# Kernel tuning notes

Measured on AMD Instinct MI355X. Metric: run time of the kernel, lower is better.

Reference implementation:

```python
import jax, jax.numpy as jnp
import numpy as np

B, T, D = 128, 32, 1024
ADA, INTER, RANK = 1024, 1024, 8
LN_EPS = 1e-5

def setup_inputs() -> dict:
    key = jax.random.key(0)
    ks = jax.random.split(key, 9)
    return {
        "x": jax.random.normal(ks[0], (B, T, D), dtype=jnp.float32),
        "ada_emb": jax.random.normal(ks[1], (B, ADA), dtype=jnp.float32),
        "base_layer": jax.random.normal(ks[2], (D, D), dtype=jnp.float32),  # torch.randn init
        "w1": jax.random.normal(ks[3], (ADA, INTER), dtype=jnp.float32) * 0.02,
        "b1": jnp.zeros((INTER,), dtype=jnp.float32),
        "w2": jax.random.normal(ks[4], (INTER, 2 * D * RANK), dtype=jnp.float32) * 0.02,
        "b2": jnp.zeros((2 * D * RANK,), dtype=jnp.float32),
        "ln_g": jnp.ones((ADA,), dtype=jnp.float32),
        "ln_b": jnp.zeros((ADA,), dtype=jnp.float32),
    }

def _layernorm(x, g, b):
    mu = jnp.mean(x, axis=-1, keepdims=True)
    var = jnp.var(x, axis=-1, keepdims=True)
    return (x - mu) * jax.lax.rsqrt(var + LN_EPS) * g + b

def reference(x, ada_emb, base_layer, w1, b1, w2, b2, ln_g, ln_b):
    b, t, d = x.shape
    # hypernetwork: cond -> per-sample LoRA factors
    ae = _layernorm(ada_emb, ln_g, ln_b)
    h = jax.nn.gelu(ae @ w1 + b1, approximate=False)  # nn.GELU is exact (erf)
    xw = h @ w2 + b2                                   # (B, 2*D*rank)
    x_a, x_b = jnp.split(xw, 2, axis=-1)
    x_a = x_a.reshape(b, d, RANK)
    x_b = x_b.reshape(b, d, RANK)
    # fused per-sample weight: base + x_a @ x_b^T  -> (B, D, D)
    layer = base_layer[None, :, :] + jnp.einsum('bdr,bkr->bdk', x_a, x_b)
    # apply shared per-sample weight to every token (equiv to repeat_interleave + bmm)
    out = jnp.einsum('btc,bco->bto', x, layer)
    return x + out  # residual=True
```

## Files before the change

### kernel.cpp

```cpp
#include <hip/hip_runtime.h>
#include <hip/hip_bf16.h>
#include <math.h>

#define BB    128
#define TT    32
#define DD    1024
#define NADA  1024
#define NINT  1024
#define NRANK 8
#define LNEPS 1e-5f
#define SPLITS 8
#define TKCH  8

using bf16x8 = __attribute__((ext_vector_type(8))) short;
using f32x4  = __attribute__((ext_vector_type(4))) float;

__device__ __forceinline__ short f2bf(float f) {
    __hip_bfloat16 h = __float2bfloat16(f);
    return *reinterpret_cast<short*>(&h);
}

__device__ __forceinline__ void async16(const void* g, void* l) {
    __builtin_amdgcn_global_load_lds(
        (const __attribute__((address_space(1))) void*)g,
        (__attribute__((address_space(3))) void*)l, 16, 0, 0);
}

__global__ __launch_bounds__(256) void ln_kernel(
    const float* __restrict__ ada, const float* __restrict__ g,
    const float* __restrict__ beta, short* __restrict__ ae)
{
    const int b = blockIdx.x;
    const float* row = ada + (size_t)b * NADA;
    float sum = 0.f, sumsq = 0.f;
    for (int i = threadIdx.x; i < NADA; i += 256) {
        float v = row[i];
        sum += v; sumsq += v * v;
    }
    #pragma unroll
    for (int off = 32; off > 0; off >>= 1) {
        sum   += __shfl_down(sum, off);
        sumsq += __shfl_down(sumsq, off);
    }
    __shared__ float s1[4], s2[4];
    const int wid = threadIdx.x >> 6, lane = threadIdx.x & 63;
    if (lane == 0) { s1[wid] = sum; s2[wid] = sumsq; }
    __syncthreads();
    if (threadIdx.x == 0) {
        float a = 0.f, c = 0.f;
        for (int i = 0; i < 4; ++i) { a += s1[i]; c += s2[i]; }
        s1[0] = a; s2[0] = c;
    }
    __syncthreads();
    const float mu  = s1[0] * (1.f / NADA);
    const float var = s2[0] * (1.f / NADA) - mu * mu;
    const float inv = rsqrtf(var + LNEPS);
    for (int i = threadIdx.x; i < NADA; i += 256) {
        ae[(size_t)b * NADA + i] = f2bf((row[i] - mu) * inv * g[i] + beta[i]);
    }
}

__global__ __launch_bounds__(256) void cast_kernel(
    const float* __restrict__ in, short* __restrict__ out)
{
    const int idx = blockIdx.x * 256 + threadIdx.x;
    float4 v = reinterpret_cast<const float4*>(in)[idx];
    short4 p;
    p.x = f2bf(v.x); p.y = f2bf(v.y); p.z = f2bf(v.z); p.w = f2bf(v.w);
    reinterpret_cast<short4*>(out)[idx] = p;
}

template <bool ADDI>
__global__ __launch_bounds__(256) void tcast_kernel(
    const float* __restrict__ in, short* __restrict__ out, int K, int N)
{
    __shared__ float t[64][68];
    const int n0 = blockIdx.x * 64, k0 = blockIdx.y * 64;
    const int tid = threadIdx.x;
    #pragma unroll
    for (int it = 0; it < 4; ++it) {
        const int idx = it * 256 + tid;
        const int r = idx >> 4, c4 = (idx & 15) * 4;
        float4 v = *(const float4*)(in + (size_t)(k0 + r) * N + n0 + c4);
        t[r][c4 + 0] = v.x; t[r][c4 + 1] = v.y;
        t[r][c4 + 2] = v.z; t[r][c4 + 3] = v.w;
    }
    __syncthreads();
    #pragma unroll
    for (int it = 0; it < 4; ++it) {
        const int idx = it * 256 + tid;
        const int rn = idx >> 4, c4 = (idx & 15) * 4;
        short4 p;
        float f0 = t[c4 + 0][rn], f1 = t[c4 + 1][rn];
        float f2 = t[c4 + 2][rn], f3 = t[c4 + 3][rn];
        if (ADDI) {
            const int n = n0 + rn;
            if (k0 + c4 + 0 == n) f0 += 1.f;
            if (k0 + c4 + 1 == n) f1 += 1.f;
            if (k0 + c4 + 2 == n) f2 += 1.f;
            if (k0 + c4 + 3 == n) f3 += 1.f;
        }
        p.x = f2bf(f0); p.y = f2bf(f1); p.z = f2bf(f2); p.w = f2bf(f3);
        *(short4*)(out + (size_t)(n0 + rn) * K + k0 + c4) = p;
    }
}

template <int BM, int BN, int WM, int WN, int EPI>
__global__ __launch_bounds__(256, 2) void mgemm(
    const short* __restrict__ A, const short* __restrict__ Bt,
    const float* __restrict__ bias, float* __restrict__ C,
    int M, int N, int K, int kLen,
    const float* __restrict__ tmat, const float* __restrict__ xw)
{
    constexpr int MT = BM / WM / 16;
    constexpr int NT = BN / WN / 16;
    constexpr int LA = BM / 64;
    constexpr int LB = BN / 64;

    __shared__ __align__(16) short As[BM * 32];
    __shared__ __align__(16) short Bs[BN * 32];
    __shared__ float tmS[(EPI == 2) ? BM * 8 : 1];
    __shared__ float xbS[(EPI == 2) ? (BM / 32) * BN * 8 : 1];

    const int bm = blockIdx.y * BM;
    const int bn = blockIdx.x * BN;
    const int kStart = blockIdx.z * kLen;
    const int tid = threadIdx.x;
    const int wave = tid >> 6, lane = tid & 63;
    const int wm0 = (wave / WN) * (BM / WM);
    const int wn0 = (wave % WN) * (BN / WN);
    const int quad = lane >> 4, r16 = lane & 15;

    if constexpr (EPI == 2) {
        const int b0 = bm >> 5;
        #pragma unroll
        for (int s = 0; s < BM * 8 / 1024; ++s) {
            const int i4 = s * 256 + tid;
            *(float4*)&tmS[i4 * 4] = *(const float4*)(tmat + (size_t)bm * 8 + i4 * 4);
        }
        const int grp = tid >> 6;
        const int inner = tid & 63;
        const float* src = xw + (size_t)(b0 + grp) * (2 * DD * NRANK) + DD * NRANK
                              + (size_t)bn * 8;
        *(float4*)&xbS[grp * BN * 8 + inner * 8]     = *(const float4*)(src + inner * 8);
        *(float4*)&xbS[grp * BN * 8 + inner * 8 + 4] = *(const float4*)(src + inner * 8 + 4);
    }

    f32x4 acc[MT][NT] = {};

    for (int kt = 0; kt < kLen; kt += 32) {
        const int k0 = kStart + kt;
        #pragma unroll
        for (int s = 0; s < LA; ++s) {
            const int c = s * 256 + tid;
            async16(A + (size_t)(bm + (c >> 2)) * K + k0 + (c & 3) * 8, &As[c * 8]);
        }
        #pragma unroll
        for (int s = 0; s < LB; ++s) {
            const int c = s * 256 + tid;
            async16(Bt + (size_t)(bn + (c >> 2)) * K + k0 + (c & 3) * 8, &Bs[c * 8]);
        }
        __syncthreads();
        bf16x8 af[MT], bfr[NT];
        #pragma unroll
        for (int i = 0; i < MT; ++i)
            af[i] = *reinterpret_cast<const bf16x8*>(&As[(wm0 + i * 16 + r16) * 32 + quad * 8]);
        #pragma unroll
        for (int j = 0; j < NT; ++j)
            bfr[j] = *reinterpret_cast<const bf16x8*>(&Bs[(wn0 + j * 16 + r16) * 32 + quad * 8]);
        #pragma unroll
        for (int i = 0; i < MT; ++i)
            #pragma unroll
            for (int j = 0; j < NT; ++j)
                acc[i][j] = __builtin_amdgcn_mfma_f32_16x16x32_bf16(
                    af[i], bfr[j], acc[i][j], 0, 0, 0);
        __syncthreads();
    }

    if constexpr (EPI == 2) {
        float xbr[NT][8];
        #pragma unroll
        for (int j = 0; j < NT; ++j) {
            const int nl = wn0 + j * 16 + r16;
            (void)nl;
        }
        #pragma unroll
        for (int i = 0; i < MT; ++i) {
            const int mlBase = wm0 + i * 16 + quad * 4;
            const int s = mlBase >> 5;
            #pragma unroll
            for (int j = 0; j < NT; ++j) {
                const int nl = wn0 + j * 16 + r16;
                #pragma unroll
                for (int rr = 0; rr < 8; ++rr)
                    xbr[j][rr] = xbS[(s * BN + nl) * 8 + rr];
            }
            #pragma unroll
            for (int r = 0; r < 4; ++r) {
                const int ml = mlBase + r;
                const int m = bm + ml;
                float t8[8];
                #pragma unroll
                for (int rr = 0; rr < 8; ++rr) t8[rr] = tmS[ml * 8 + rr];
                #pragma unroll
                for (int j = 0; j < NT; ++j) {
                    const int n = bn + wn0 + j * 16 + r16;
                    float v = acc[i][j][r];
                    #pragma unroll
                    for (int rr = 0; rr < 8; ++rr) v += t8[rr] * xbr[j][rr];
                    C[(size_t)m * N + n] = v;
                }
            }
        }
    } else {
        #pragma unroll
        for (int i = 0; i < MT; ++i) {
            #pragma unroll
            for (int r = 0; r < 4; ++r) {
                const int m = bm + wm0 + i * 16 + quad * 4 + r;
                #pragma unroll
                for (int j = 0; j < NT; ++j) {
                    const int n = bn + wn0 + j * 16 + r16;
                    float v = acc[i][j][r];
                    if (EPI == 0) {
                        C[((size_t)blockIdx.z * M + m) * N + n] = v;
                    } else {
                        C[(size_t)m * N + n] = v + bias[n];
                    }
                }
            }
        }
    }
}

__global__ __launch_bounds__(256) void combine_gelu(
    const float* __restrict__ part, const float* __restrict__ b1,
    short* __restrict__ h)
{
    const int idx = blockIdx.x * 256 + threadIdx.x;
    float s = b1[idx & (NINT - 1)];
    #pragma unroll
    for (int z = 0; z < SPLITS; ++z) s += part[(size_t)z * BB * NINT + idx];
    s = 0.5f * s * (1.f + erff(s * 0.70710678118654752f));
    h[idx] = f2bf(s);
}

__global__ __launch_bounds__(256) void tpart_kernel(
    const float* __restrict__ x, const float* __restrict__ xw,
    float* __restrict__ tp)
{
    __shared__ float xa[(DD / TKCH) * NRANK];
    const int b = blockIdx.x, ch = blockIdx.y;
    const float* src = xw + (size_t)b * (2 * DD * NRANK) + (size_t)ch * (DD / TKCH) * NRANK;
    float4 v = *(const float4*)(src + threadIdx.x * 4);
    *(float4*)(xa + threadIdx.x * 4) = v;
    __syncthreads();
    const int m = threadIdx.x >> 3;
    const int r = threadIdx.x & 7;
    const float* xrow = x + ((size_t)b * TT + m) * DD + ch * (DD / TKCH);
    float accv = 0.f;
    #pragma unroll 4
    for (int c = 0; c < DD / TKCH; c += 4) {
        float4 xr = *(const float4*)(xrow + c);
        accv += xr.x * xa[(c + 0) * NRANK + r];
        accv += xr.y * xa[(c + 1) * NRANK + r];
        accv += xr.z * xa[(c + 2) * NRANK + r];
        accv += xr.w * xa[(c + 3) * NRANK + r];
    }
    tp[((size_t)ch * BB * TT + (size_t)b * TT + m) * NRANK + r] = accv;
}

__global__ __launch_bounds__(256) void tcomb_kernel(
    const float* __restrict__ tp, float* __restrict__ tm)
{
    const int i = blockIdx.x * 256 + threadIdx.x;
    float s = 0.f;
    #pragma unroll
    for (int ch = 0; ch < TKCH; ++ch) s += tp[(size_t)ch * BB * TT * NRANK + i];
    tm[i] = s;
}

extern "C" void kernel_launch(void* const* d_in, const int* in_sizes, int n_in,
                              void* d_out, int out_size, void* d_ws, size_t ws_size,
                              hipStream_t stream)
{
    const float* x    = (const float*)d_in[0];
    const float* ada  = (const float*)d_in[1];
    const float* base = (const float*)d_in[2];
    const float* w1   = (const float*)d_in[3];
    const float* b1   = (const float*)d_in[4];
    const float* w2   = (const float*)d_in[5];
    const float* b2   = (const float*)d_in[6];
    const float* lng  = (const float*)d_in[7];
    const float* lnb  = (const float*)d_in[8];
    float* out = (float*)d_out;

    char* w = (char*)d_ws;
    short* x_bf  = (short*)w;  w += (size_t)8 << 20;
    short* w2t   = (short*)w;  w += (size_t)32 << 20;
    short* w1t   = (short*)w;  w += (size_t)2 << 20;
    short* baset = (short*)w;  w += (size_t)2 << 20;
    short* ae_bf = (short*)w;  w += (size_t)256 << 10;
    short* h_bf  = (short*)w;  w += (size_t)256 << 10;
    float* xw    = (float*)w;  w += (size_t)8 << 20;
    float* tm    = (float*)w;  w += (size_t)128 << 10;
    float* part  = (float*)w;
    float* tp    = part;

    cast_kernel<<<BB * TT * DD / 1024, 256, 0, stream>>>(x, x_bf);
    tcast_kernel<false><<<dim3(NINT / 64, NADA / 64), 256, 0, stream>>>(w1, w1t, NADA, NINT);
    tcast_kernel<true><<<dim3(DD / 64, DD / 64), 256, 0, stream>>>(base, baset, DD, DD);
    tcast_kernel<false><<<dim3(2 * DD * NRANK / 64, NINT / 64), 256, 0, stream>>>(
        w2, w2t, NINT, 2 * DD * NRANK);
    ln_kernel<<<BB, 256, 0, stream>>>(ada, lng, lnb, ae_bf);
    mgemm<64, 64, 2, 2, 0><<<dim3(NINT / 64, BB / 64, SPLITS), 256, 0, stream>>>(
        ae_bf, w1t, nullptr, part, BB, NINT, NADA, NADA / SPLITS, nullptr, nullptr);
    combine_gelu<<<BB * NINT / 256, 256, 0, stream>>>(part, b1, h_bf);
    mgemm<64, 64, 2, 2, 1><<<dim3(2 * DD * NRANK / 64, BB / 64, 1), 256, 0, stream>>>(
        h_bf, w2t, b2, xw, BB, 2 * DD * NRANK, NINT, NINT, nullptr, nullptr);
    tpart_kernel<<<dim3(BB, TKCH), 256, 0, stream>>>(x, xw, tp);
    tcomb_kernel<<<BB * TT * NRANK / 256, 256, 0, stream>>>(tp, tm);
    mgemm<128, 64, 2, 2, 2><<<dim3(DD / 64, BB * TT / 128, 1), 256, 0, stream>>>(
        x_bf, baset, nullptr, out, BB * TT, DD, DD, DD, tm, xw);
}
```

Baseline: 197.8 us.

## Fuse prep kernels, drop split-K for first GEMM, fold combines into GEMM epilogues

Merges the x cast, three transposed weight casts and layernorm into a single block-indexed prep kernel. The first GEMM no longer uses split-K; bias and exact GELU are applied in its epilogue, so the combine_gelu pass goes away. The tcomb reduction is moved into the prologue of the final GEMM, which sums the eight partials itself. The aim is fewer launches and less intermediate traffic, at the cost of the first GEMM running only 32 blocks over the full K.

```diff
diff --git a/kernel.cpp b/kernel.cpp
--- a/kernel.cpp
+++ b/kernel.cpp
@@ -9,7 +9,6 @@
 #define NINT  1024
 #define NRANK 8
 #define LNEPS 1e-5f
-#define SPLITS 8
 #define TKCH  8
 
 using bf16x8 = __attribute__((ext_vector_type(8))) short;
@@ -26,57 +25,11 @@
         (__attribute__((address_space(3))) void*)l, 16, 0, 0);
 }
 
-__global__ __launch_bounds__(256) void ln_kernel(
-    const float* __restrict__ ada, const float* __restrict__ g,
-    const float* __restrict__ beta, short* __restrict__ ae)
-{
-    const int b = blockIdx.x;
-    const float* row = ada + (size_t)b * NADA;
-    float sum = 0.f, sumsq = 0.f;
-    for (int i = threadIdx.x; i < NADA; i += 256) {
-        float v = row[i];
-        sum += v; sumsq += v * v;
-    }
-    #pragma unroll
-    for (int off = 32; off > 0; off >>= 1) {
-        sum   += __shfl_down(sum, off);
-        sumsq += __shfl_down(sumsq, off);
-    }
-    __shared__ float s1[4], s2[4];
-    const int wid = threadIdx.x >> 6, lane = threadIdx.x & 63;
-    if (lane == 0) { s1[wid] = sum; s2[wid] = sumsq; }
-    __syncthreads();
-    if (threadIdx.x == 0) {
-        float a = 0.f, c = 0.f;
-        for (int i = 0; i < 4; ++i) { a += s1[i]; c += s2[i]; }
-        s1[0] = a; s2[0] = c;
-    }
-    __syncthreads();
-    const float mu  = s1[0] * (1.f / NADA);
-    const float var = s2[0] * (1.f / NADA) - mu * mu;
-    const float inv = rsqrtf(var + LNEPS);
-    for (int i = threadIdx.x; i < NADA; i += 256) {
-        ae[(size_t)b * NADA + i] = f2bf((row[i] - mu) * inv * g[i] + beta[i]);
-    }
-}
-
-__global__ __launch_bounds__(256) void cast_kernel(
-    const float* __restrict__ in, short* __restrict__ out)
-{
-    const int idx = blockIdx.x * 256 + threadIdx.x;
-    float4 v = reinterpret_cast<const float4*>(in)[idx];
-    short4 p;
-    p.x = f2bf(v.x); p.y = f2bf(v.y); p.z = f2bf(v.z); p.w = f2bf(v.w);
-    reinterpret_cast<short4*>(out)[idx] = p;
-}
-
-template <bool ADDI>
-__global__ __launch_bounds__(256) void tcast_kernel(
-    const float* __restrict__ in, short* __restrict__ out, int K, int N)
-{
-    __shared__ float t[64][68];
-    const int n0 = blockIdx.x * 64, k0 = blockIdx.y * 64;
-    const int tid = threadIdx.x;
+__device__ __forceinline__ void tcast_tile(
+    const float* __restrict__ in, short* __restrict__ out, int K, int N,
+    int bx, int by, bool addI, int tid, float (*t)[68])
+{
+    const int n0 = bx * 64, k0 = by * 64;
     #pragma unroll
     for (int it = 0; it < 4; ++it) {
         const int idx = it * 256 + tid;
@@ -90,18 +43,81 @@
     for (int it = 0; it < 4; ++it) {
         const int idx = it * 256 + tid;
         const int rn = idx >> 4, c4 = (idx & 15) * 4;
-        short4 p;
         float f0 = t[c4 + 0][rn], f1 = t[c4 + 1][rn];
         float f2 = t[c4 + 2][rn], f3 = t[c4 + 3][rn];
-        if (ADDI) {
+        if (addI) {
             const int n = n0 + rn;
             if (k0 + c4 + 0 == n) f0 += 1.f;
             if (k0 + c4 + 1 == n) f1 += 1.f;
             if (k0 + c4 + 2 == n) f2 += 1.f;
             if (k0 + c4 + 3 == n) f3 += 1.f;
         }
+        short4 p;
         p.x = f2bf(f0); p.y = f2bf(f1); p.z = f2bf(f2); p.w = f2bf(f3);
         *(short4*)(out + (size_t)(n0 + rn) * K + k0 + c4) = p;
+    }
+}
+
+__global__ __launch_bounds__(256) void prep_kernel(
+    const float* __restrict__ x, const float* __restrict__ w1,
+    const float* __restrict__ base, const float* __restrict__ w2,
+    const float* __restrict__ ada, const float* __restrict__ lng,
+    const float* __restrict__ lnb,
+    short* __restrict__ x_bf, short* __restrict__ w1t,
+    short* __restrict__ baset, short* __restrict__ w2t,
+    short* __restrict__ ae_bf)
+{
+    __shared__ float t[64][68];
+    const int bid = blockIdx.x, tid = threadIdx.x;
+
+    if (bid < 4096) {
+        tcast_tile(w2, w2t, NINT, 2 * DD * NRANK, bid & 255, bid >> 8, false, tid, t);
+    } else if (bid < 6144) {
+        const int b = bid - 4096;
+        const int i0 = b * 512 + tid;
+        float4 v0 = reinterpret_cast<const float4*>(x)[i0];
+        float4 v1 = reinterpret_cast<const float4*>(x)[i0 + 256];
+        short4 p0, p1;
+        p0.x = f2bf(v0.x); p0.y = f2bf(v0.y); p0.z = f2bf(v0.z); p0.w = f2bf(v0.w);
+        p1.x = f2bf(v1.x); p1.y = f2bf(v1.y); p1.z = f2bf(v1.z); p1.w = f2bf(v1.w);
+        reinterpret_cast<short4*>(x_bf)[i0] = p0;
+        reinterpret_cast<short4*>(x_bf)[i0 + 256] = p1;
+    } else if (bid < 6400) {
+        const int b = bid - 6144;
+        tcast_tile(w1, w1t, NADA, NINT, b & 15, b >> 4, false, tid, t);
+    } else if (bid < 6656) {
+        const int b = bid - 6400;
+        tcast_tile(base, baset, DD, DD, b & 15, b >> 4, true, tid, t);
+    } else {
+        const int b = bid - 6656;
+        const float* row = ada + (size_t)b * NADA;
+        float sum = 0.f, sumsq = 0.f;
+        for (int i = tid; i < NADA; i += 256) {
+            float v = row[i];
+            sum += v; sumsq += v * v;
+        }
+        #pragma unroll
+        for (int off = 32; off > 0; off >>= 1) {
+            sum   += __shfl_down(sum, off);
+            sumsq += __shfl_down(sumsq, off);
+        }
+        float* s1 = &t[0][0];
+        float* s2 = &t[1][0];
+        const int wid = tid >> 6, lane = tid & 63;
+        if (lane == 0) { s1[wid] = sum; s2[wid] = sumsq; }
+        __syncthreads();
+        if (tid == 0) {
+            float a = 0.f, c = 0.f;
+            for (int i = 0; i < 4; ++i) { a += s1[i]; c += s2[i]; }
+            s1[0] = a; s2[0] = c;
+        }
+        __syncthreads();
+        const float mu  = s1[0] * (1.f / NADA);
+        const float var = s2[0] * (1.f / NADA) - mu * mu;
+        const float inv = rsqrtf(var + LNEPS);
+        for (int i = tid; i < NADA; i += 256) {
+            ae_bf[(size_t)b * NADA + i] = f2bf((row[i] - mu) * inv * lng[i] + lnb[i]);
+        }
     }
 }
 
@@ -110,7 +126,7 @@
     const short* __restrict__ A, const short* __restrict__ Bt,
     const float* __restrict__ bias, float* __restrict__ C,
     int M, int N, int K, int kLen,
-    const float* __restrict__ tmat, const float* __restrict__ xw)
+    const float* __restrict__ tp, const float* __restrict__ xw)
 {
     constexpr int MT = BM / WM / 16;
     constexpr int NT = BN / WN / 16;
@@ -124,7 +140,6 @@
 
     const int bm = blockIdx.y * BM;
     const int bn = blockIdx.x * BN;
-    const int kStart = blockIdx.z * kLen;
     const int tid = threadIdx.x;
     const int wave = tid >> 6, lane = tid & 63;
     const int wm0 = (wave / WN) * (BM / WM);
@@ -132,12 +147,15 @@
     const int quad = lane >> 4, r16 = lane & 15;
 
     if constexpr (EPI == 2) {
+        float4 a = {0.f, 0.f, 0.f, 0.f};
+        #pragma unroll
+        for (int ch = 0; ch < TKCH; ++ch) {
+            float4 v = *(const float4*)(tp + (size_t)ch * BB * TT * NRANK
+                                           + (size_t)bm * 8 + tid * 4);
+            a.x += v.x; a.y += v.y; a.z += v.z; a.w += v.w;
+        }
+        *(float4*)&tmS[tid * 4] = a;
         const int b0 = bm >> 5;
-        #pragma unroll
-        for (int s = 0; s < BM * 8 / 1024; ++s) {
-            const int i4 = s * 256 + tid;
-            *(float4*)&tmS[i4 * 4] = *(const float4*)(tmat + (size_t)bm * 8 + i4 * 4);
-        }
         const int grp = tid >> 6;
         const int inner = tid & 63;
         const float* src = xw + (size_t)(b0 + grp) * (2 * DD * NRANK) + DD * NRANK
@@ -148,8 +166,7 @@
 
     f32x4 acc[MT][NT] = {};
 
-    for (int kt = 0; kt < kLen; kt += 32) {
-        const int k0 = kStart + kt;
+    for (int k0 = 0; k0 < kLen; k0 += 32) {
         #pragma unroll
         for (int s = 0; s < LA; ++s) {
             const int c = s * 256 + tid;
@@ -179,11 +196,6 @@
 
     if constexpr (EPI == 2) {
         float xbr[NT][8];
-        #pragma unroll
-        for (int j = 0; j < NT; ++j) {
-            const int nl = wn0 + j * 16 + r16;
-            (void)nl;
-        }
         #pragma unroll
         for (int i = 0; i < MT; ++i) {
             const int mlBase = wm0 + i * 16 + quad * 4;
@@ -221,28 +233,17 @@
                 #pragma unroll
                 for (int j = 0; j < NT; ++j) {
                     const int n = bn + wn0 + j * 16 + r16;
-                    float v = acc[i][j][r];
-                    if (EPI == 0) {
-                        C[((size_t)blockIdx.z * M + m) * N + n] = v;
+                    float v = acc[i][j][r] + bias[n];
+                    if (EPI == 1) {
+                        C[(size_t)m * N + n] = v;
                     } else {
-                        C[(size_t)m * N + n] = v + bias[n];
+                        v = 0.5f * v * (1.f + erff(v * 0.70710678118654752f));
+                        ((short*)C)[(size_t)m * N + n] = f2bf(v);
                     }
                 }
             }
         }
     }
-}
-
-__global__ __launch_bounds__(256) void combine_gelu(
-    const float* __restrict__ part, const float* __restrict__ b1,
-    short* __restrict__ h)
-{
-    const int idx = blockIdx.x * 256 + threadIdx.x;
-    float s = b1[idx & (NINT - 1)];
-    #pragma unroll
-    for (int z = 0; z < SPLITS; ++z) s += part[(size_t)z * BB * NINT + idx];
-    s = 0.5f * s * (1.f + erff(s * 0.70710678118654752f));
-    h[idx] = f2bf(s);
 }
 
 __global__ __launch_bounds__(256) void tpart_kernel(
@@ -270,16 +271,6 @@
     tp[((size_t)ch * BB * TT + (size_t)b * TT + m) * NRANK + r] = accv;
 }
 
-__global__ __launch_bounds__(256) void tcomb_kernel(
-    const float* __restrict__ tp, float* __restrict__ tm)
-{
-    const int i = blockIdx.x * 256 + threadIdx.x;
-    float s = 0.f;
-    #pragma unroll
-    for (int ch = 0; ch < TKCH; ++ch) s += tp[(size_t)ch * BB * TT * NRANK + i];
-    tm[i] = s;
-}
-
 extern "C" void kernel_launch(void* const* d_in, const int* in_sizes, int n_in,
                               void* d_out, int out_size, void* d_ws, size_t ws_size,
                               hipStream_t stream)
@@ -303,23 +294,15 @@
     short* ae_bf = (short*)w;  w += (size_t)256 << 10;
     short* h_bf  = (short*)w;  w += (size_t)256 << 10;
     float* xw    = (float*)w;  w += (size_t)8 << 20;
-    float* tm    = (float*)w;  w += (size_t)128 << 10;
-    float* part  = (float*)w;
-    float* tp    = part;
-
-    cast_kernel<<<BB * TT * DD / 1024, 256, 0, stream>>>(x, x_bf);
-    tcast_kernel<false><<<dim3(NINT / 64, NADA / 64), 256, 0, stream>>>(w1, w1t, NADA, NINT);
-    tcast_kernel<true><<<dim3(DD / 64, DD / 64), 256, 0, stream>>>(base, baset, DD, DD);
-    tcast_kernel<false><<<dim3(2 * DD * NRANK / 64, NINT / 64), 256, 0, stream>>>(
-        w2, w2t, NINT, 2 * DD * NRANK);
-    ln_kernel<<<BB, 256, 0, stream>>>(ada, lng, lnb, ae_bf);
-    mgemm<64, 64, 2, 2, 0><<<dim3(NINT / 64, BB / 64, SPLITS), 256, 0, stream>>>(
-        ae_bf, w1t, nullptr, part, BB, NINT, NADA, NADA / SPLITS, nullptr, nullptr);
-    combine_gelu<<<BB * NINT / 256, 256, 0, stream>>>(part, b1, h_bf);
-    mgemm<64, 64, 2, 2, 1><<<dim3(2 * DD * NRANK / 64, BB / 64, 1), 256, 0, stream>>>(
+    float* tp    = (float*)w;
+
+    prep_kernel<<<6784, 256, 0, stream>>>(
+        x, w1, base, w2, ada, lng, lnb, x_bf, w1t, baset, w2t, ae_bf);
+    mgemm<64, 64, 2, 2, 3><<<dim3(NINT / 64, BB / 64), 256, 0, stream>>>(
+        ae_bf, w1t, b1, (float*)h_bf, BB, NINT, NADA, NADA, nullptr, nullptr);
+    mgemm<64, 64, 2, 2, 1><<<dim3(2 * DD * NRANK / 64, BB / 64), 256, 0, stream>>>(
         h_bf, w2t, b2, xw, BB, 2 * DD * NRANK, NINT, NINT, nullptr, nullptr);
     tpart_kernel<<<dim3(BB, TKCH), 256, 0, stream>>>(x, xw, tp);
-    tcomb_kernel<<<BB * TT * NRANK / 256, 256, 0, stream>>>(tp, tm);
-    mgemm<128, 64, 2, 2, 2><<<dim3(DD / 64, BB * TT / 128, 1), 256, 0, stream>>>(
-        x_bf, baset, nullptr, out, BB * TT, DD, DD, DD, tm, xw);
-}
+    mgemm<128, 64, 2, 2, 2><<<dim3(DD / 64, BB * TT / 128), 256, 0, stream>>>(
+        x_bf, baset, nullptr, out, BB * TT, DD, DD, DD, tp, xw);
+}
```

Result: no change. 196.4 us (-0.7%).
